# Optimization experiments

Measured on AMD Instinct MI355X. Metric: run time of the kernel, lower is better.

## Reference

```python
import jax, jax.numpy as jnp
import numpy as np

HEAD_SIZE = 64
N_EMBD = 1024
B, T = 8, 2048


def setup_inputs() -> dict:
    key = jax.random.key(0)
    kx, kk, kq, kv = jax.random.split(key, 4)
    scale = 1.0 / np.sqrt(N_EMBD)
    return {
        "x": jax.random.normal(kx, (B, T, N_EMBD), dtype=jnp.float32),
        "Wk": jax.random.normal(kk, (N_EMBD, HEAD_SIZE), dtype=jnp.float32) * scale,
        "Wq": jax.random.normal(kq, (N_EMBD, HEAD_SIZE), dtype=jnp.float32) * scale,
        "Wv": jax.random.normal(kv, (N_EMBD, HEAD_SIZE), dtype=jnp.float32) * scale,
    }


def reference(x, Wk, Wq, Wv):
    # x: [B, T, E]; W*: [E, H] (equivalent to x @ nn.Linear.weight.T)
    k = jnp.einsum("bte,eh->bth", x, Wk)
    q = jnp.einsum("bte,eh->bth", x, Wq)
    v = jnp.einsum("bte,eh->bth", x, Wv)
    head_size = k.shape[-1]
    # scores: [B, T, T]
    wei = jnp.einsum("bqh,bkh->bqk", q, k) * (head_size ** -0.5)
    t = x.shape[1]
    causal = jnp.tril(jnp.ones((t, t), dtype=bool))  # [T, T]
    wei = jnp.where(causal, wei, -jnp.inf)
    wei = jax.nn.softmax(wei, axis=-1)
    # dropout p=0.0 -> identity
    out = jnp.einsum("bqk,bkh->bqh", wei, v)
    return out
```

## Files before the change

kernel.cpp:

```cpp
#include <hip/hip_runtime.h>
#include <cstdint>

#define BATCH 8
#define T_SEQ 2048
#define E_DIM 1024
#define H_DIM 64
#define BT (BATCH * T_SEQ)

typedef __attribute__((ext_vector_type(8))) short bf16x8;
typedef __attribute__((ext_vector_type(4))) float f32x4;

static __device__ __forceinline__ short f2bf(float f) {
    uint32_t b = __float_as_uint(f);
    b += 0x7fffu + ((b >> 16) & 1u);
    return (short)(b >> 16);
}

#define Q_OFF   0
#define K_OFF   (BT * H_DIM)
#define VT_OFF  (2 * BT * H_DIM)
#define WT_OFF  (3 * BT * H_DIM)

static __device__ __forceinline__ void glds16(const void* g, void* l) {
    __builtin_amdgcn_global_load_lds(
        (const __attribute__((address_space(1))) void*)g,
        (__attribute__((address_space(3))) void*)l, 16, 0, 0);
}


__global__ void wt_prep_frag(const float* __restrict__ Wk, const float* __restrict__ Wq,
                             const float* __restrict__ Wv, short* __restrict__ wtb) {
    int gid = blockIdx.x * 256 + threadIdx.x;
    int lane = gid & 63;
    int kt = (gid >> 6) & 31;
    int f = gid >> 11;
    int m = f >> 2, ct = f & 3;
    int col = (ct << 4) | (lane & 15);
    int k0 = (kt << 5) | (((lane >> 4) & 3) << 3);
    const float* W = (m == 0) ? Wk : ((m == 1) ? Wq : Wv);
    bf16x8 v;
    #pragma unroll
    for (int e = 0; e < 8; ++e) v[e] = f2bf(W[(size_t)(k0 + e) * H_DIM + col]);
    *reinterpret_cast<bf16x8*>(wtb + (size_t)gid * 8) = v;
}

__global__ __launch_bounds__(256, 2) void proj_fused(
    const float* __restrict__ x, const short* __restrict__ wtb,
    short* __restrict__ qo, short* __restrict__ kb_, short* __restrict__ vb_)
{
    __shared__ __align__(16) short Bs[2][24 * 512];
    __shared__ __align__(16) short Xs[2][4 * 64 * 8];

    const int tid  = threadIdx.x;
    const int lane = tid & 63;
    const int w    = tid >> 6;
    const int kh   = w >> 1;
    const int rtl  = w & 1;
    const int rt_g = blockIdx.x * 2 + rtl;
    const int row0 = blockIdx.x * 32;

    const f32x4 z4 = {0.f, 0.f, 0.f, 0.f};
    f32x4 acc[12];
    #pragma unroll
    for (int f = 0; f < 12; ++f) acc[f] = z4;

    #define STAGE_B(buf, s)                                                            \
        {                                                                              \
            _Pragma("unroll")                                                          \
            for (int ci = 0; ci < 6; ++ci) {                                           \
                int c = w * 6 + ci;                                                    \
                int f = c % 12, khc = c / 12;                                          \
                const short* src = wtb + (((size_t)f * 32 + khc * 16 + (s)) * 64 + lane) * 8; \
                glds16(src, &Bs[buf][c * 512]);                                        \
            }                                                                          \
        }

    #define STAGE_A(buf, s)                                                            \
        {                                                                              \
            int row = tid >> 3, k8 = tid & 7;                                          \
            int khs = k8 >> 2, j = k8 & 3;                                             \
            const float* xp = x + (size_t)(row0 + row) * E_DIM + khs * 512 + (s) * 32 + j * 8; \
            float4 a = *reinterpret_cast<const float4*>(xp);                           \
            float4 b = *reinterpret_cast<const float4*>(xp + 4);                       \
            bf16x8 v;                                                                  \
            v[0] = f2bf(a.x); v[1] = f2bf(a.y); v[2] = f2bf(a.z); v[3] = f2bf(a.w);    \
            v[4] = f2bf(b.x); v[5] = f2bf(b.y); v[6] = f2bf(b.z); v[7] = f2bf(b.w);    \
            int c = ((row >> 4) << 1) | khs;                                           \
            int slot = (j << 4) | (row & 15);                                          \
            *reinterpret_cast<bf16x8*>(&Xs[buf][(c * 64 + slot) * 8]) = v;             \
        }

    STAGE_B(0, 0);
    STAGE_A(0, 0);
    __syncthreads();

    const int ac = ((rtl << 1) | kh) * 64;
    int buf = 0;
    for (int s = 0; s < 16; ++s) {
        if (s < 15) {
            STAGE_B(buf ^ 1, s + 1);
            STAGE_A(buf ^ 1, s + 1);
        }
        bf16x8 afc = *reinterpret_cast<const bf16x8*>(&Xs[buf][(ac + lane) * 8]);
        #pragma unroll
        for (int f = 0; f < 12; ++f) {
            bf16x8 bfv = *reinterpret_cast<const bf16x8*>(&Bs[buf][(kh * 12 + f) * 512 + lane * 8]);
            acc[f] = __builtin_amdgcn_mfma_f32_16x16x32_bf16(afc, bfv, acc[f], 0, 0, 0);
        }
        __syncthreads();
        buf ^= 1;
    }

    float* mrg = reinterpret_cast<float*>(&Bs[0][0]);
    if (kh == 1) {
        #pragma unroll
        for (int f = 0; f < 12; ++f)
            *reinterpret_cast<f32x4*>(mrg + ((size_t)(rtl * 12 + f) * 64 + lane) * 4) = acc[f];
    }
    __syncthreads();
    if (kh == 0) {
        const int col16 = lane & 15, rowb = (lane >> 4) << 2;
        const int R0 = rt_g * 16 + rowb;
        #pragma unroll
        for (int m = 0; m < 3; ++m) {
            #pragma unroll
            for (int ct = 0; ct < 4; ++ct) {
                int f = m * 4 + ct;
                f32x4 v = acc[f];
                f32x4 o = *reinterpret_cast<const f32x4*>(mrg + ((size_t)(rtl * 12 + f) * 64 + lane) * 4);
                v.x += o.x; v.y += o.y; v.z += o.z; v.w += o.w;
                int C = (ct << 4) | col16;
                #pragma unroll
                for (int i = 0; i < 4; ++i) {
                    int R = R0 + i;
                    int b = R >> 11, tok = R & 2047, tt = tok >> 6;
                    if (m == 1) {
                        qo[(size_t)R * H_DIM + C] = f2bf(v[i] * 0.125f);
                    } else if (m == 0) {
                        int ctk = (tok >> 4) & 3, lnk = (tok & 15) | (((C >> 3) & 3) << 4);
                        int sk = C >> 5, ek = C & 7;
                        kb_[(((((size_t)b * 32 + tt) * 4 + ctk) * 2 + sk) * 64 + lnk) * 8 + ek] = f2bf(v[i]);
                    } else {
                        int sv = (tok >> 5) & 1, gv = (tok >> 3) & 3, ev = tok & 7;
                        int dtv = C >> 4, lnv = (C & 15) | (gv << 4);
                        vb_[(((((size_t)b * 32 + tt) * 4 + dtv) * 2 + sv) * 64 + lnv) * 8 + ev] = f2bf(v[i]);
                    }
                }
            }
        }
    }
}

#define SWZ(row, off) ((off) ^ (((row) & 7) << 3))

__global__ __launch_bounds__(512, 4) void attn3(
    const short* __restrict__ q, const short* __restrict__ kb,
    const short* __restrict__ vb, float* __restrict__ out)
{
    __shared__ __align__(16) short Ps[8][16 * 64];
    __shared__ float Og[4][16][64];
    __shared__ float Mg[4][16], Lg[4][16];

    const int tid  = threadIdx.x;
    const int lane = tid & 63;
    const int w    = tid >> 6;
    const int band = w & 1;
    const int kq   = w >> 1;
    const int bb   = blockIdx.x & 7;
    const int j    = blockIdx.x >> 3;
    const int p    = (j < 32) ? (63 - j) : (j - 32);

    const int q0 = p << 5;
    const int Nt = (p >> 1) + 1;

    const int qrowA = q0 + (band << 4) + (lane & 15);
    bf16x8 qf[2];
    #pragma unroll
    for (int s = 0; s < 2; ++s)
        qf[s] = *reinterpret_cast<const bf16x8*>(
            q + (size_t)(bb * T_SEQ + qrowA) * H_DIM + s * 32 + ((lane >> 4) << 3));

    const f32x4 z4 = {0.f, 0.f, 0.f, 0.f};
    float mreg[4] = {-1e30f, -1e30f, -1e30f, -1e30f};
    float lreg[4] = {0.f, 0.f, 0.f, 0.f};
    f32x4 oacc[4] = {z4, z4, z4, z4};

    const short* kbb = kb + (size_t)bb * 32 * 4096;
    const short* vbb = vb + (size_t)bb * 32 * 4096;

    for (int t = kq; t < Nt; t += 4) {
        const short* kt = kbb + (size_t)t * 4096 + lane * 8;
        f32x4 sacc[4] = {z4, z4, z4, z4};
        #pragma unroll
        for (int s = 0; s < 2; ++s)
            #pragma unroll
            for (int ct = 0; ct < 4; ++ct) {
                bf16x8 bfv = *reinterpret_cast<const bf16x8*>(kt + (ct * 2 + s) * 512);
                sacc[ct] = __builtin_amdgcn_mfma_f32_16x16x32_bf16(qf[s], bfv, sacc[ct], 0, 0, 0);
            }
        const short* vt_ = vbb + (size_t)t * 4096 + lane * 8;
        bf16x8 Vc[8];
        #pragma unroll
        for (int u = 0; u < 8; ++u)
            Vc[u] = *reinterpret_cast<const bf16x8*>(vt_ + u * 512);
        if (t == Nt - 1) {
            int qgb = q0 + (band << 4) + ((lane >> 4) << 2);
            #pragma unroll
            for (int ct = 0; ct < 4; ++ct) {
                int kg = t * 64 + (ct << 4) + (lane & 15);
                #pragma unroll
                for (int i = 0; i < 4; ++i)
                    if (kg > qgb + i) sacc[ct][i] = -1e30f;
            }
        }
        #pragma unroll
        for (int i = 0; i < 4; ++i) {
            float s0 = sacc[0][i], s1 = sacc[1][i], s2 = sacc[2][i], s3 = sacc[3][i];
            float tmax = fmaxf(fmaxf(s0, s1), fmaxf(s2, s3));
            tmax = fmaxf(tmax, __shfl_xor(tmax, 1));
            tmax = fmaxf(tmax, __shfl_xor(tmax, 2));
            tmax = fmaxf(tmax, __shfl_xor(tmax, 4));
            tmax = fmaxf(tmax, __shfl_xor(tmax, 8));
            float mnew = fmaxf(mreg[i], tmax);
            float sc = __expf(mreg[i] - mnew);
            mreg[i] = mnew;
            float p0 = __expf(s0 - mnew), p1 = __expf(s1 - mnew);
            float p2 = __expf(s2 - mnew), p3 = __expf(s3 - mnew);
            float ps = p0 + p1 + p2 + p3;
            ps += __shfl_xor(ps, 1); ps += __shfl_xor(ps, 2);
            ps += __shfl_xor(ps, 4); ps += __shfl_xor(ps, 8);
            lreg[i] = lreg[i] * sc + ps;
            oacc[0][i] *= sc; oacc[1][i] *= sc; oacc[2][i] *= sc; oacc[3][i] *= sc;
            int rq = ((lane >> 4) << 2) + i;
            short* pr = &Ps[w][rq * 64];
            pr[SWZ(rq, (0 << 4) + (lane & 15))] = f2bf(p0);
            pr[SWZ(rq, (1 << 4) + (lane & 15))] = f2bf(p1);
            pr[SWZ(rq, (2 << 4) + (lane & 15))] = f2bf(p2);
            pr[SWZ(rq, (3 << 4) + (lane & 15))] = f2bf(p3);
        }
        int qa = lane & 15;
        #pragma unroll
        for (int dt = 0; dt < 4; ++dt)
            #pragma unroll
            for (int s = 0; s < 2; ++s) {
                int koff = s * 32 + ((lane >> 4) << 3);
                bf16x8 af = *reinterpret_cast<const bf16x8*>(&Ps[w][qa * 64 + SWZ(qa, koff)]);
                oacc[dt] = __builtin_amdgcn_mfma_f32_16x16x32_bf16(af, Vc[dt * 2 + s], oacc[dt], 0, 0, 0);
            }
    }

    __syncthreads();
    if (kq >= 2) {
        int slot = (band << 1) | (kq - 2);
        #pragma unroll
        for (int i = 0; i < 4; ++i) {
            int rq = ((lane >> 4) << 2) + i;
            #pragma unroll
            for (int dt = 0; dt < 4; ++dt)
                Og[slot][rq][(dt << 4) + (lane & 15)] = oacc[dt][i];
            if ((lane & 15) == 0) { Mg[slot][rq] = mreg[i]; Lg[slot][rq] = lreg[i]; }
        }
    }
    __syncthreads();
    if (kq < 2) {
        int slot = (band << 1) | kq;
        #pragma unroll
        for (int i = 0; i < 4; ++i) {
            int rq = ((lane >> 4) << 2) + i;
            float m1 = Mg[slot][rq], l1 = Lg[slot][rq];
            float mm = fmaxf(mreg[i], m1);
            float f0 = __expf(mreg[i] - mm), f1 = __expf(m1 - mm);
            mreg[i] = mm;
            lreg[i] = lreg[i] * f0 + l1 * f1;
            #pragma unroll
            for (int dt = 0; dt < 4; ++dt)
                oacc[dt][i] = oacc[dt][i] * f0 + Og[slot][rq][(dt << 4) + (lane & 15)] * f1;
        }
    }
    __syncthreads();
    if (kq == 1) {
        int slot = (band << 1) | 1;
        #pragma unroll
        for (int i = 0; i < 4; ++i) {
            int rq = ((lane >> 4) << 2) + i;
            #pragma unroll
            for (int dt = 0; dt < 4; ++dt)
                Og[slot][rq][(dt << 4) + (lane & 15)] = oacc[dt][i];
            if ((lane & 15) == 0) { Mg[slot][rq] = mreg[i]; Lg[slot][rq] = lreg[i]; }
        }
    }
    __syncthreads();
    if (kq == 0) {
        int slot = (band << 1) | 1;
        #pragma unroll
        for (int i = 0; i < 4; ++i) {
            int rq = ((lane >> 4) << 2) + i;
            float m1 = Mg[slot][rq], l1 = Lg[slot][rq];
            float mm = fmaxf(mreg[i], m1);
            float f0 = __expf(mreg[i] - mm), f1 = __expf(m1 - mm);
            float l  = lreg[i] * f0 + l1 * f1;
            float inv = 1.f / l;
            size_t orow = (size_t)(bb * T_SEQ + q0 + (band << 4) + rq) * H_DIM;
            #pragma unroll
            for (int dt = 0; dt < 4; ++dt) {
                float ov = oacc[dt][i] * f0 + Og[slot][rq][(dt << 4) + (lane & 15)] * f1;
                out[orow + (dt << 4) + (lane & 15)] = ov * inv;
            }
        }
    }
}

extern "C" void kernel_launch(void* const* d_in, const int* in_sizes, int n_in,
                              void* d_out, int out_size, void* d_ws, size_t ws_size,
                              hipStream_t stream) {
    const float* x  = (const float*)d_in[0];
    const float* Wk = (const float*)d_in[1];
    const float* Wq = (const float*)d_in[2];
    const float* Wv = (const float*)d_in[3];
    float* out = (float*)d_out;

    short* ws  = (short*)d_ws;
    short* qb  = ws + Q_OFF;
    short* kbp = ws + K_OFF;
    short* vbp = ws + VT_OFF;
    short* wtb = ws + WT_OFF;

    wt_prep_frag<<<96, 256, 0, stream>>>(Wk, Wq, Wv, wtb);
    proj_fused<<<BT / 32, 256, 0, stream>>>(x, wtb, qb, kbp, vbp);
    attn3<<<512, 512, 0, stream>>>(qb, kbp, vbp, out);
}
```

Before: 53.63 us.

## Rewrite projection and attention kernels with direct loads and register prefetch

The projection kernel drops the LDS double-buffer staging and reads x and the weight fragments straight from global memory into registers, using packed hardware bf16 conversion. Each block now covers 64 rows with 512 threads. The attention kernel moves to 16-row query tiles with 4 waves per block and twice as many blocks. It prefetches the next K/V tile into registers while current MFMAs run, and raises wave priority around the MFMA sections. This is meant to cut LDS and sync overhead and hide memory latency, at the cost of more register pressure and redundant global reads of the weights.

```diff
diff --git a/kernel.cpp b/kernel.cpp
--- a/kernel.cpp
+++ b/kernel.cpp
@@ -16,16 +16,19 @@
     return (short)(b >> 16);
 }
 
+static __device__ __forceinline__ bf16x8 cvt8(float4 a, float4 b) {
+    union { bf16x8 v; uint32_t u[4]; } r;
+    asm("v_cvt_pk_bf16_f32 %0, %1, %2" : "=v"(r.u[0]) : "v"(a.x), "v"(a.y));
+    asm("v_cvt_pk_bf16_f32 %0, %1, %2" : "=v"(r.u[1]) : "v"(a.z), "v"(a.w));
+    asm("v_cvt_pk_bf16_f32 %0, %1, %2" : "=v"(r.u[2]) : "v"(b.x), "v"(b.y));
+    asm("v_cvt_pk_bf16_f32 %0, %1, %2" : "=v"(r.u[3]) : "v"(b.z), "v"(b.w));
+    return r.v;
+}
+
 #define Q_OFF   0
 #define K_OFF   (BT * H_DIM)
 #define VT_OFF  (2 * BT * H_DIM)
 #define WT_OFF  (3 * BT * H_DIM)
-
-static __device__ __forceinline__ void glds16(const void* g, void* l) {
-    __builtin_amdgcn_global_load_lds(
-        (const __attribute__((address_space(1))) void*)g,
-        (__attribute__((address_space(3))) void*)l, 16, 0, 0);
-}
 
 
 __global__ void wt_prep_frag(const float* __restrict__ Wk, const float* __restrict__ Wq,
@@ -44,91 +47,61 @@
     *reinterpret_cast<bf16x8*>(wtb + (size_t)gid * 8) = v;
 }
 
-__global__ __launch_bounds__(256, 2) void proj_fused(
+__global__ __launch_bounds__(512, 2) void proj4(
     const float* __restrict__ x, const short* __restrict__ wtb,
     short* __restrict__ qo, short* __restrict__ kb_, short* __restrict__ vb_)
 {
-    __shared__ __align__(16) short Bs[2][24 * 512];
-    __shared__ __align__(16) short Xs[2][4 * 64 * 8];
+    __shared__ float MM[4][12 * 256];
 
     const int tid  = threadIdx.x;
     const int lane = tid & 63;
     const int w    = tid >> 6;
-    const int kh   = w >> 1;
-    const int rtl  = w & 1;
-    const int rt_g = blockIdx.x * 2 + rtl;
-    const int row0 = blockIdx.x * 32;
+    const int rt   = w & 3;
+    const int kh   = w >> 2;
+    const int row0 = blockIdx.x * 64;
 
     const f32x4 z4 = {0.f, 0.f, 0.f, 0.f};
     f32x4 acc[12];
     #pragma unroll
     for (int f = 0; f < 12; ++f) acc[f] = z4;
 
-    #define STAGE_B(buf, s)                                                            \
-        {                                                                              \
-            _Pragma("unroll")                                                          \
-            for (int ci = 0; ci < 6; ++ci) {                                           \
-                int c = w * 6 + ci;                                                    \
-                int f = c % 12, khc = c / 12;                                          \
-                const short* src = wtb + (((size_t)f * 32 + khc * 16 + (s)) * 64 + lane) * 8; \
-                glds16(src, &Bs[buf][c * 512]);                                        \
-            }                                                                          \
-        }
-
-    #define STAGE_A(buf, s)                                                            \
-        {                                                                              \
-            int row = tid >> 3, k8 = tid & 7;                                          \
-            int khs = k8 >> 2, j = k8 & 3;                                             \
-            const float* xp = x + (size_t)(row0 + row) * E_DIM + khs * 512 + (s) * 32 + j * 8; \
-            float4 a = *reinterpret_cast<const float4*>(xp);                           \
-            float4 b = *reinterpret_cast<const float4*>(xp + 4);                       \
-            bf16x8 v;                                                                  \
-            v[0] = f2bf(a.x); v[1] = f2bf(a.y); v[2] = f2bf(a.z); v[3] = f2bf(a.w);    \
-            v[4] = f2bf(b.x); v[5] = f2bf(b.y); v[6] = f2bf(b.z); v[7] = f2bf(b.w);    \
-            int c = ((row >> 4) << 1) | khs;                                           \
-            int slot = (j << 4) | (row & 15);                                          \
-            *reinterpret_cast<bf16x8*>(&Xs[buf][(c * 64 + slot) * 8]) = v;             \
-        }
-
-    STAGE_B(0, 0);
-    STAGE_A(0, 0);
-    __syncthreads();
-
-    const int ac = ((rtl << 1) | kh) * 64;
-    int buf = 0;
+    const float* xp0 = x + (size_t)(row0 + rt * 16 + (lane & 15)) * E_DIM
+                         + (kh << 9) + ((lane >> 4) << 3);
+    const short* wp0 = wtb + (size_t)(kh << 4) * 512 + lane * 8;
+
+    #pragma unroll 4
     for (int s = 0; s < 16; ++s) {
-        if (s < 15) {
-            STAGE_B(buf ^ 1, s + 1);
-            STAGE_A(buf ^ 1, s + 1);
-        }
-        bf16x8 afc = *reinterpret_cast<const bf16x8*>(&Xs[buf][(ac + lane) * 8]);
+        float4 a = *reinterpret_cast<const float4*>(xp0 + s * 32);
+        float4 b = *reinterpret_cast<const float4*>(xp0 + s * 32 + 4);
+        bf16x8 af = cvt8(a, b);
+        const short* wp = wp0 + (size_t)s * 512;
         #pragma unroll
         for (int f = 0; f < 12; ++f) {
-            bf16x8 bfv = *reinterpret_cast<const bf16x8*>(&Bs[buf][(kh * 12 + f) * 512 + lane * 8]);
-            acc[f] = __builtin_amdgcn_mfma_f32_16x16x32_bf16(afc, bfv, acc[f], 0, 0, 0);
-        }
-        __syncthreads();
-        buf ^= 1;
-    }
-
-    float* mrg = reinterpret_cast<float*>(&Bs[0][0]);
+            bf16x8 bfv = *reinterpret_cast<const bf16x8*>(wp + (size_t)f * 16384);
+            acc[f] = __builtin_amdgcn_mfma_f32_16x16x32_bf16(af, bfv, acc[f], 0, 0, 0);
+        }
+    }
+
     if (kh == 1) {
         #pragma unroll
         for (int f = 0; f < 12; ++f)
-            *reinterpret_cast<f32x4*>(mrg + ((size_t)(rtl * 12 + f) * 64 + lane) * 4) = acc[f];
+            *reinterpret_cast<f32x4*>(&MM[rt][(f * 64 + lane) * 4]) = acc[f];
     }
     __syncthreads();
     if (kh == 0) {
+        #pragma unroll
+        for (int f = 0; f < 12; ++f) {
+            f32x4 o = *reinterpret_cast<const f32x4*>(&MM[rt][(f * 64 + lane) * 4]);
+            acc[f].x += o.x; acc[f].y += o.y; acc[f].z += o.z; acc[f].w += o.w;
+        }
         const int col16 = lane & 15, rowb = (lane >> 4) << 2;
-        const int R0 = rt_g * 16 + rowb;
+        const int R0 = row0 + rt * 16 + rowb;
         #pragma unroll
         for (int m = 0; m < 3; ++m) {
             #pragma unroll
             for (int ct = 0; ct < 4; ++ct) {
                 int f = m * 4 + ct;
                 f32x4 v = acc[f];
-                f32x4 o = *reinterpret_cast<const f32x4*>(mrg + ((size_t)(rtl * 12 + f) * 64 + lane) * 4);
-                v.x += o.x; v.y += o.y; v.z += o.z; v.w += o.w;
                 int C = (ct << 4) | col16;
                 #pragma unroll
                 for (int i = 0; i < 4; ++i) {
@@ -153,32 +126,30 @@
 
 #define SWZ(row, off) ((off) ^ (((row) & 7) << 3))
 
-__global__ __launch_bounds__(512, 4) void attn3(
+__global__ __launch_bounds__(256, 3) void attn4(
     const short* __restrict__ q, const short* __restrict__ kb,
     const short* __restrict__ vb, float* __restrict__ out)
 {
-    __shared__ __align__(16) short Ps[8][16 * 64];
-    __shared__ float Og[4][16][64];
-    __shared__ float Mg[4][16], Lg[4][16];
+    __shared__ __align__(16) short Ps[4][16 * 64];
+    __shared__ float Og[2][16][64];
+    __shared__ float Mg[2][16], Lg[2][16];
 
     const int tid  = threadIdx.x;
     const int lane = tid & 63;
     const int w    = tid >> 6;
-    const int band = w & 1;
-    const int kq   = w >> 1;
-    const int bb   = blockIdx.x & 7;
-    const int j    = blockIdx.x >> 3;
-    const int p    = (j < 32) ? (63 - j) : (j - 32);
-
-    const int q0 = p << 5;
-    const int Nt = (p >> 1) + 1;
-
-    const int qrowA = q0 + (band << 4) + (lane & 15);
+    const int bb   = blockIdx.x >> 7;
+    const int j    = blockIdx.x & 127;
+    const int p    = (j < 64) ? (127 - j) : (j - 64);
+
+    const int q0 = p << 4;
+    const int Nt = (p >> 2) + 1;
+
     bf16x8 qf[2];
+    const int qrow = q0 + (lane & 15);
     #pragma unroll
     for (int s = 0; s < 2; ++s)
         qf[s] = *reinterpret_cast<const bf16x8*>(
-            q + (size_t)(bb * T_SEQ + qrowA) * H_DIM + s * 32 + ((lane >> 4) << 3));
+            q + (size_t)(bb * T_SEQ + qrow) * H_DIM + s * 32 + ((lane >> 4) << 3));
 
     const f32x4 z4 = {0.f, 0.f, 0.f, 0.f};
     float mreg[4] = {-1e30f, -1e30f, -1e30f, -1e30f};
@@ -188,23 +159,34 @@
     const short* kbb = kb + (size_t)bb * 32 * 4096;
     const short* vbb = vb + (size_t)bb * 32 * 4096;
 
-    for (int t = kq; t < Nt; t += 4) {
-        const short* kt = kbb + (size_t)t * 4096 + lane * 8;
+    bf16x8 Kc[8], Vc[8];
+    {
+        const short* kt0 = kbb + (size_t)w * 4096 + lane * 8;
+        const short* vt0 = vbb + (size_t)w * 4096 + lane * 8;
+        #pragma unroll
+        for (int u = 0; u < 8; ++u) {
+            Kc[u] = *reinterpret_cast<const bf16x8*>(kt0 + u * 512);
+            Vc[u] = *reinterpret_cast<const bf16x8*>(vt0 + u * 512);
+        }
+    }
+
+    for (int t = w; t < Nt; t += 4) {
         f32x4 sacc[4] = {z4, z4, z4, z4};
+        __builtin_amdgcn_s_setprio(1);
         #pragma unroll
         for (int s = 0; s < 2; ++s)
             #pragma unroll
-            for (int ct = 0; ct < 4; ++ct) {
-                bf16x8 bfv = *reinterpret_cast<const bf16x8*>(kt + (ct * 2 + s) * 512);
-                sacc[ct] = __builtin_amdgcn_mfma_f32_16x16x32_bf16(qf[s], bfv, sacc[ct], 0, 0, 0);
-            }
-        const short* vt_ = vbb + (size_t)t * 4096 + lane * 8;
-        bf16x8 Vc[8];
-        #pragma unroll
-        for (int u = 0; u < 8; ++u)
-            Vc[u] = *reinterpret_cast<const bf16x8*>(vt_ + u * 512);
+            for (int ct = 0; ct < 4; ++ct)
+                sacc[ct] = __builtin_amdgcn_mfma_f32_16x16x32_bf16(qf[s], Kc[ct * 2 + s], sacc[ct], 0, 0, 0);
+        __builtin_amdgcn_s_setprio(0);
+        if (t + 4 < Nt) {
+            const short* ktn = kbb + (size_t)(t + 4) * 4096 + lane * 8;
+            #pragma unroll
+            for (int u = 0; u < 8; ++u)
+                Kc[u] = *reinterpret_cast<const bf16x8*>(ktn + u * 512);
+        }
         if (t == Nt - 1) {
-            int qgb = q0 + (band << 4) + ((lane >> 4) << 2);
+            int qgb = q0 + ((lane >> 4) << 2);
             #pragma unroll
             for (int ct = 0; ct < 4; ++ct) {
                 int kg = t * 64 + (ct << 4) + (lane & 15);
@@ -239,6 +221,7 @@
             pr[SWZ(rq, (3 << 4) + (lane & 15))] = f2bf(p3);
         }
         int qa = lane & 15;
+        __builtin_amdgcn_s_setprio(1);
         #pragma unroll
         for (int dt = 0; dt < 4; ++dt)
             #pragma unroll
@@ -247,11 +230,18 @@
                 bf16x8 af = *reinterpret_cast<const bf16x8*>(&Ps[w][qa * 64 + SWZ(qa, koff)]);
                 oacc[dt] = __builtin_amdgcn_mfma_f32_16x16x32_bf16(af, Vc[dt * 2 + s], oacc[dt], 0, 0, 0);
             }
-    }
-
-    __syncthreads();
-    if (kq >= 2) {
-        int slot = (band << 1) | (kq - 2);
+        __builtin_amdgcn_s_setprio(0);
+        if (t + 4 < Nt) {
+            const short* vtn = vbb + (size_t)(t + 4) * 4096 + lane * 8;
+            #pragma unroll
+            for (int u = 0; u < 8; ++u)
+                Vc[u] = *reinterpret_cast<const bf16x8*>(vtn + u * 512);
+        }
+    }
+
+    __syncthreads();
+    if (w >= 2) {
+        int slot = w - 2;
         #pragma unroll
         for (int i = 0; i < 4; ++i) {
             int rq = ((lane >> 4) << 2) + i;
@@ -262,8 +252,8 @@
         }
     }
     __syncthreads();
-    if (kq < 2) {
-        int slot = (band << 1) | kq;
+    if (w < 2) {
+        int slot = w;
         #pragma unroll
         for (int i = 0; i < 4; ++i) {
             int rq = ((lane >> 4) << 2) + i;
@@ -278,32 +268,30 @@
         }
     }
     __syncthreads();
-    if (kq == 1) {
-        int slot = (band << 1) | 1;
+    if (w == 1) {
         #pragma unroll
         for (int i = 0; i < 4; ++i) {
             int rq = ((lane >> 4) << 2) + i;
             #pragma unroll
             for (int dt = 0; dt < 4; ++dt)
-                Og[slot][rq][(dt << 4) + (lane & 15)] = oacc[dt][i];
-            if ((lane & 15) == 0) { Mg[slot][rq] = mreg[i]; Lg[slot][rq] = lreg[i]; }
-        }
-    }
-    __syncthreads();
-    if (kq == 0) {
-        int slot = (band << 1) | 1;
-        #pragma unroll
-        for (int i = 0; i < 4; ++i) {
-            int rq = ((lane >> 4) << 2) + i;
-            float m1 = Mg[slot][rq], l1 = Lg[slot][rq];
+                Og[1][rq][(dt << 4) + (lane & 15)] = oacc[dt][i];
+            if ((lane & 15) == 0) { Mg[1][rq] = mreg[i]; Lg[1][rq] = lreg[i]; }
+        }
+    }
+    __syncthreads();
+    if (w == 0) {
+        #pragma unroll
+        for (int i = 0; i < 4; ++i) {
+            int rq = ((lane >> 4) << 2) + i;
+            float m1 = Mg[1][rq], l1 = Lg[1][rq];
             float mm = fmaxf(mreg[i], m1);
             float f0 = __expf(mreg[i] - mm), f1 = __expf(m1 - mm);
             float l  = lreg[i] * f0 + l1 * f1;
             float inv = 1.f / l;
-            size_t orow = (size_t)(bb * T_SEQ + q0 + (band << 4) + rq) * H_DIM;
+            size_t orow = (size_t)(bb * T_SEQ + q0 + rq) * H_DIM;
             #pragma unroll
             for (int dt = 0; dt < 4; ++dt) {
-                float ov = oacc[dt][i] * f0 + Og[slot][rq][(dt << 4) + (lane & 15)] * f1;
+                float ov = oacc[dt][i] * f0 + Og[1][rq][(dt << 4) + (lane & 15)] * f1;
                 out[orow + (dt << 4) + (lane & 15)] = ov * inv;
             }
         }
@@ -326,6 +314,6 @@
     short* wtb = ws + WT_OFF;
 
     wt_prep_frag<<<96, 256, 0, stream>>>(Wk, Wq, Wv, wtb);
-    proj_fused<<<BT / 32, 256, 0, stream>>>(x, wtb, qb, kbp, vbp);
-    attn3<<<512, 512, 0, stream>>>(qb, kbp, vbp, out);
-}
+    proj4<<<BT / 64, 512, 0, stream>>>(x, wtb, qb, kbp, vbp);
+    attn4<<<BATCH * 128, 256, 0, stream>>>(qb, kbp, vbp, out);
+}
```

Result: slower. 84.95 us (+58.4%).
